# Optimization experiments

Measured on AMD Instinct MI355X. Metric: run time of the kernel, lower is better.

## Reference

```python
import jax, jax.numpy as jnp
import numpy as np

B, S, D = 2, 2048, 1024
H = 16
HD = D // H  # head_dim = 64
EPS = 1e-5


def _layernorm(x, g, b):
    mu = jnp.mean(x, axis=-1, keepdims=True)
    var = jnp.mean(jnp.square(x - mu), axis=-1, keepdims=True)
    return (x - mu) * jax.lax.rsqrt(var + EPS) * g + b


def setup_inputs() -> dict:
    key = jax.random.key(0)
    ks = jax.random.split(key, 6)
    # Xavier-normal-ish init for projection weights (torch Linear layout: [out, in])
    std = float(np.sqrt(2.0 / (D + D)))
    return {
        "query": jax.random.normal(ks[0], (B, S, D), dtype=jnp.float32),
        "q_w": jax.random.normal(ks[1], (D, D), dtype=jnp.float32) * std,
        "q_b": jnp.zeros((D,), jnp.float32),
        "k_w": jax.random.normal(ks[2], (D, D), dtype=jnp.float32) * std,
        "k_b": jnp.zeros((D,), jnp.float32),
        "v_w": jax.random.normal(ks[3], (D, D), dtype=jnp.float32) * std,
        "v_b": jnp.zeros((D,), jnp.float32),
        "o_w": jax.random.normal(ks[4], (D, D), dtype=jnp.float32) * std,
        "o_b": jnp.zeros((D,), jnp.float32),
        "q_ln_g": jnp.ones((HD,), jnp.float32),
        "q_ln_b": jnp.zeros((HD,), jnp.float32),
        "k_ln_g": jnp.ones((HD,), jnp.float32),
        "k_ln_b": jnp.zeros((HD,), jnp.float32),
    }


def reference(query, q_w, q_b, k_w, k_b, v_w, v_b, o_w, o_b,
              q_ln_g, q_ln_b, k_ln_g, k_ln_b) -> jnp.ndarray:
    # Self-attention: key = value = query
    q = query @ q_w.T + q_b           # [B, S, D]
    k = query @ k_w.T + k_b
    v = query @ v_w.T + v_b
    q = q.reshape(B, S, H, HD)
    k = k.reshape(B, S, H, HD)
    v = v.reshape(B, S, H, HD)
    # Per-head QK LayerNorm (ViT-22B stabilization)
    q = _layernorm(q, q_ln_g, q_ln_b)
    k = _layernorm(k, k_ln_g, k_ln_b)
    scale = 1.0 / jnp.sqrt(jnp.asarray(HD, q.dtype))
    attn = jnp.einsum("bqhd,bkhd->bhqk", q, k) * scale  # [B, H, Sq, Skv]
    attn = jax.nn.softmax(attn, axis=-1)
    out = jnp.einsum("bhqk,bkhd->bqhd", attn, v)        # [B, Sq, H, HD]
    out = out.reshape(B, S, D)
    return out @ o_w.T + o_b
```

## Files before the change

kernel.cpp:

```cpp
#include <hip/hip_runtime.h>
#include <hip/hip_bf16.h>

typedef float f32x4 __attribute__((ext_vector_type(4)));
typedef __bf16 bf16x8 __attribute__((ext_vector_type(8)));
typedef unsigned short ushort8 __attribute__((ext_vector_type(8)));
typedef unsigned short ushort4e __attribute__((ext_vector_type(4)));

#define SEQ 2048
#define LOG2E 1.4426950408889634f

__device__ __forceinline__ unsigned short f2bf(float f) {
    unsigned int u = __builtin_bit_cast(unsigned int, f);
    unsigned int r = (u + 0x7FFFu + ((u >> 16) & 1u)) >> 16;
    return (unsigned short)r;
}

__device__ __forceinline__ void gload_lds16(const unsigned short* g, unsigned short* l) {
    __builtin_amdgcn_global_load_lds(
        (const __attribute__((address_space(1))) unsigned int*)g,
        (__attribute__((address_space(3))) unsigned int*)l, 16, 0, 0);
}

__global__ __launch_bounds__(256) void conv_bf16(
    const float* __restrict__ s0, const float* __restrict__ s1,
    const float* __restrict__ s2, const float* __restrict__ s3,
    const float* __restrict__ s4,
    unsigned short* __restrict__ d0, unsigned short* __restrict__ d1,
    unsigned short* __restrict__ d2, unsigned short* __restrict__ d3,
    unsigned short* __restrict__ d4)
{
    const int seg = blockIdx.y;
    const float* s = seg == 0 ? s0 : seg == 1 ? s1 : seg == 2 ? s2 : seg == 3 ? s3 : s4;
    unsigned short* d = seg == 0 ? d0 : seg == 1 ? d1 : seg == 2 ? d2 : seg == 3 ? d3 : d4;
    const int n = seg == 0 ? (4096 * 1024) : (1024 * 1024);
    const int i = (blockIdx.x * 256 + threadIdx.x) * 8;
    if (i >= n) return;
    float4 a = *(const float4*)(s + i);
    float4 b = *(const float4*)(s + i + 4);
    ushort8 o;
    o[0] = f2bf(a.x); o[1] = f2bf(a.y); o[2] = f2bf(a.z); o[3] = f2bf(a.w);
    o[4] = f2bf(b.x); o[5] = f2bf(b.y); o[6] = f2bf(b.z); o[7] = f2bf(b.w);
    *(ushort8*)(d + i) = o;
}

__global__ __launch_bounds__(256) void gemm_bf16(
    const unsigned short* __restrict__ A,
    const unsigned short* __restrict__ W0, const unsigned short* __restrict__ W1,
    const unsigned short* __restrict__ W2,
    const float* __restrict__ b0, const float* __restrict__ b1, const float* __restrict__ b2,
    const float* __restrict__ ln_g0, const float* __restrict__ ln_b0,
    const float* __restrict__ ln_g1, const float* __restrict__ ln_b1,
    unsigned short* __restrict__ qn, unsigned short* __restrict__ kn,
    unsigned short* __restrict__ vt,
    float* __restrict__ Cout, int fixed_mode)
{
    const int z = fixed_mode < 0 ? (int)blockIdx.z : fixed_mode;
    const unsigned short* W = (z == 1) ? W1 : (z == 2) ? W2 : W0;
    const float* bias = (z == 1) ? b1 : (z == 2) ? b2 : b0;

    const int bm = blockIdx.y * 128;
    const int bn = blockIdx.x * 128;

    __shared__ unsigned short As[128 * 64];
    __shared__ unsigned short Bs[128 * 64];

    const int t    = threadIdx.x;
    const int lane = t & 63;
    const int wid  = t >> 6;
    const int l15  = lane & 15;
    const int lhi  = lane >> 4;
    const int wm   = (wid >> 1) * 64;
    const int wn   = (wid & 1) * 64;

    const int schunk = (lane & 7) ^ ((lane >> 3) & 7);
    const unsigned short* Ag = A + (size_t)(bm + (lane >> 3)) * 1024 + schunk * 8;
    const unsigned short* Wg = W + (size_t)(bn + (lane >> 3)) * 1024 + schunk * 8;

    f32x4 acc[4][4];
#pragma unroll
    for (int i = 0; i < 4; ++i)
#pragma unroll
        for (int j = 0; j < 4; ++j) acc[i][j] = (f32x4)0.f;

#pragma unroll 1
    for (int kt = 0; kt < 1024; kt += 64) {
        __syncthreads();
#pragma unroll
        for (int c = 0; c < 4; ++c) {
            const int ch = wid * 4 + c;
            gload_lds16(Ag + (size_t)ch * 8 * 1024 + kt, &As[ch * 512]);
            gload_lds16(Wg + (size_t)ch * 8 * 1024 + kt, &Bs[ch * 512]);
        }
        __syncthreads();
#pragma unroll
        for (int kk = 0; kk < 2; ++kk) {
            const int rchunk = ((kk * 4 + lhi) ^ (l15 & 7)) * 8;
            bf16x8 af[4], bw[4];
#pragma unroll
            for (int mi = 0; mi < 4; ++mi)
                af[mi] = __builtin_bit_cast(bf16x8,
                    *(const ushort8*)(&As[(wm + mi * 16 + l15) * 64 + rchunk]));
#pragma unroll
            for (int ni = 0; ni < 4; ++ni)
                bw[ni] = __builtin_bit_cast(bf16x8,
                    *(const ushort8*)(&Bs[(wn + ni * 16 + l15) * 64 + rchunk]));
#pragma unroll
            for (int mi = 0; mi < 4; ++mi)
#pragma unroll
                for (int ni = 0; ni < 4; ++ni)
                    acc[mi][ni] = __builtin_amdgcn_mfma_f32_16x16x32_bf16(af[mi], bw[ni], acc[mi][ni], 0, 0, 0);
        }
    }
    __syncthreads();

    if (z == 3) {
#pragma unroll
        for (int ni = 0; ni < 4; ++ni) {
            const int col = bn + wn + ni * 16 + l15;
            const float bv = bias[col];
#pragma unroll
            for (int mi = 0; mi < 4; ++mi) {
                const int row = bm + wm + mi * 16 + lhi * 4;
#pragma unroll
                for (int r = 0; r < 4; ++r)
                    Cout[(size_t)(row + r) * 1024 + col] = acc[mi][ni][r] + bv;
            }
        }
        return;
    }

    unsigned short* stg = ((wid & 2) ? Bs : As) + (wid & 1) * 4096;
    const int h = (bn + wn) >> 6;

    if (z == 2) {
        float biasv[4];
#pragma unroll
        for (int ni = 0; ni < 4; ++ni) biasv[ni] = bias[bn + wn + ni * 16 + l15];
#pragma unroll
        for (int mi = 0; mi < 4; ++mi)
#pragma unroll
            for (int ni = 0; ni < 4; ++ni)
#pragma unroll
                for (int r = 0; r < 4; ++r)
                    stg[(ni * 16 + l15) * 64 + 32 * (mi >> 1) + lhi * 8 + 2 * r + (mi & 1)] =
                        f2bf(acc[mi][ni][r] + biasv[ni]);
        __builtin_amdgcn_s_waitcnt(0);
        const int srow0 = bm + wm;
        const int b = srow0 >> 11, sbase = srow0 & 2047;
#pragma unroll
        for (int i = 0; i < 8; ++i) {
            const int dl = i * 8 + (lane >> 3);
            const ushort8 v = *(const ushort8*)(&stg[dl * 64 + (((lane & 7) ^ (dl & 7)) * 8)]);
            *(ushort8*)(&vt[((size_t)((b * 16 + h) * 64 + dl)) * 2048 + sbase + (lane & 7) * 8]) = v;
        }
        return;
    }

    const float* g  = (z == 0) ? ln_g0 : ln_g1;
    const float* bb = (z == 0) ? ln_b0 : ln_b1;
    unsigned short* outp = (z == 0) ? qn : kn;
    const float scale = (z == 0) ? 0.125f * LOG2E : 1.0f;
    const int sxor = (z == 1) ? 7 : 0;
    float gv[4], bbv[4], biasv[4];
#pragma unroll
    for (int ni = 0; ni < 4; ++ni) {
        const int d = ni * 16 + l15;
        gv[ni] = g[d]; bbv[ni] = bb[d]; biasv[ni] = bias[bn + wn + d];
    }
#pragma unroll
    for (int mi = 0; mi < 4; ++mi) {
#pragma unroll
        for (int r = 0; r < 4; ++r) {
            float x0 = acc[mi][0][r] + biasv[0];
            float x1 = acc[mi][1][r] + biasv[1];
            float x2 = acc[mi][2][r] + biasv[2];
            float x3 = acc[mi][3][r] + biasv[3];
            float sum = (x0 + x1) + (x2 + x3);
#pragma unroll
            for (int off = 1; off < 16; off <<= 1) sum += __shfl_xor(sum, off);
            const float mean = sum * (1.f / 64.f);
            const float d0 = x0 - mean, d1 = x1 - mean, d2 = x2 - mean, d3 = x3 - mean;
            float vs = (d0 * d0 + d1 * d1) + (d2 * d2 + d3 * d3);
#pragma unroll
            for (int off = 1; off < 16; off <<= 1) vs += __shfl_xor(vs, off);
            const float rstd = rsqrtf(vs * (1.f / 64.f) + 1e-5f);
            const int rl = mi * 16 + lhi * 4 + r;
            stg[rl * 64 +  0 + l15] = f2bf((d0 * rstd * gv[0] + bbv[0]) * scale);
            stg[rl * 64 + 16 + l15] = f2bf((d1 * rstd * gv[1] + bbv[1]) * scale);
            stg[rl * 64 + 32 + l15] = f2bf((d2 * rstd * gv[2] + bbv[2]) * scale);
            stg[rl * 64 + 48 + l15] = f2bf((d3 * rstd * gv[3] + bbv[3]) * scale);
        }
    }
    __builtin_amdgcn_s_waitcnt(0);
#pragma unroll
    for (int i = 0; i < 8; ++i) {
        const int rl  = i * 8 + (lane >> 3);
        const int srow = bm + wm + rl;
        const int b = srow >> 11, s = srow & 2047;
        const ushort8 v = *(const ushort8*)(&stg[rl * 64 + (((lane & 7) ^ (rl & sxor)) * 8)]);
        *(ushort8*)(&outp[((size_t)((b * 16 + h) * 2048 + s)) * 64 + (lane & 7) * 8]) = v;
    }
}

__global__ __launch_bounds__(512, 4) void attn(
    const unsigned short* __restrict__ qn, const unsigned short* __restrict__ kn,
    const unsigned short* __restrict__ vt, unsigned short* __restrict__ o)
{
    __shared__ unsigned short Ks[4][64 * 64];
    __shared__ unsigned short Vs[4][64 * 64];
    __shared__ unsigned short Ps[128 * 64];

    const int tid  = threadIdx.x;
    const int lane = tid & 63;
    const int w    = tid >> 6;
    const int l15  = lane & 15;
    const int lhi  = lane >> 4;

    const int bh = blockIdx.x;
    const int q0 = blockIdx.y * 128;

    const unsigned short* qrp = qn + ((size_t)bh * SEQ + q0 + w * 16 + l15) * 64 + lhi * 8;
    const bf16x8 aq0 = __builtin_bit_cast(bf16x8, *(const ushort8*)(qrp));
    const bf16x8 aq1 = __builtin_bit_cast(bf16x8, *(const ushort8*)(qrp + 32));

    const unsigned short* kg = kn + ((size_t)bh * SEQ + w * 8 + (lane >> 3)) * 64 + (lane & 7) * 8;
    const unsigned short* vg = vt + ((size_t)bh * 64 + w * 8 + (lane >> 3)) * 2048 + (lane & 7) * 8;

    f32x4 oacc[4];
#pragma unroll
    for (int nd = 0; nd < 4; ++nd) oacc[nd] = (f32x4)0.f;
    float l_part[4];
#pragma unroll
    for (int i = 0; i < 4; ++i) l_part[i] = 0.f;
    f32x4 mneg = (f32x4)100.f;

    f32x4 sacc[4];

    auto QK = [&](const unsigned short* kb) {
        __builtin_amdgcn_s_setprio(1);
#pragma unroll
        for (int ni = 0; ni < 4; ++ni) {
            const int krow = ni * 16 + l15;
            const bf16x8 bk = __builtin_bit_cast(bf16x8,
                *(const ushort8*)(&kb[krow * 64 + ((lhi ^ (krow & 7)) * 8)]));
            sacc[ni] = __builtin_amdgcn_mfma_f32_16x16x32_bf16(aq0, bk, mneg, 0, 0, 0);
        }
#pragma unroll
        for (int ni = 0; ni < 4; ++ni) {
            const int krow = ni * 16 + l15;
            const bf16x8 bk = __builtin_bit_cast(bf16x8,
                *(const ushort8*)(&kb[krow * 64 + (((4 + lhi) ^ (krow & 7)) * 8)]));
            sacc[ni] = __builtin_amdgcn_mfma_f32_16x16x32_bf16(aq1, bk, sacc[ni], 0, 0, 0);
        }
        __builtin_amdgcn_s_setprio(0);
    };

    gload_lds16(kg,                    &Ks[0][w * 512]);
    gload_lds16(vg,                    &Vs[0][w * 512]);
    gload_lds16(kg + (size_t)64 * 64,  &Ks[1][w * 512]);
    gload_lds16(vg + 64,               &Vs[1][w * 512]);
    __builtin_amdgcn_sched_barrier(0);
    asm volatile("s_waitcnt vmcnt(2)" ::: "memory");
    asm volatile("s_barrier" ::: "memory");
    QK(&Ks[0][0]);

#pragma unroll 4
    for (int t = 0; t < 32; ++t) {
        if (t < 30) {
            gload_lds16(kg + (size_t)(t + 2) * 64 * 64, &Ks[(t + 2) & 3][w * 512]);
            gload_lds16(vg + (t + 2) * 64,              &Vs[(t + 2) & 3][w * 512]);
        }
        __builtin_amdgcn_sched_barrier(0);

        float tmax[4];
#pragma unroll
        for (int r = 0; r < 4; ++r)
            tmax[r] = fmaxf(fmaxf(sacc[0][r], sacc[1][r]), fmaxf(sacc[2][r], sacc[3][r]));
        const float dmax = fmaxf(fmaxf(tmax[0], tmax[1]), fmaxf(tmax[2], tmax[3]));
        if (!__all(dmax <= 8.0f)) {
#pragma unroll
            for (int r = 0; r < 4; ++r) {
                float tm = tmax[r];
#pragma unroll
                for (int off = 1; off < 16; off <<= 1) tm = fmaxf(tm, __shfl_xor(tm, off));
                const float delta = fmaxf(tm, 0.f);
                const float alpha = __builtin_amdgcn_exp2f(-delta);
                mneg[r] -= delta;
                l_part[r] *= alpha;
#pragma unroll
                for (int nd = 0; nd < 4; ++nd) oacc[nd][r] *= alpha;
#pragma unroll
                for (int ni = 0; ni < 4; ++ni) sacc[ni][r] -= delta;
            }
        }
#pragma unroll
        for (int r = 0; r < 4; ++r) {
            const float p0 = __builtin_amdgcn_exp2f(sacc[0][r]);
            const float p1 = __builtin_amdgcn_exp2f(sacc[1][r]);
            const float p2 = __builtin_amdgcn_exp2f(sacc[2][r]);
            const float p3 = __builtin_amdgcn_exp2f(sacc[3][r]);
            l_part[r] += (p0 + p1) + (p2 + p3);
            unsigned int pk0, pk1;
            asm("v_cvt_pk_bf16_f32 %0, %1, %2" : "=v"(pk0) : "v"(p0), "v"(p1));
            asm("v_cvt_pk_bf16_f32 %0, %1, %2" : "=v"(pk1) : "v"(p2), "v"(p3));
            const int prow = w * 16 + lhi * 4 + r;
            const int rs7  = prow & 7;
            *(unsigned int*)(&Ps[prow * 64 + (((l15 >> 2) ^ rs7) * 8) + 2 * (l15 & 3)]) = pk0;
            *(unsigned int*)(&Ps[prow * 64 + (((4 + (l15 >> 2)) ^ rs7) * 8) + 2 * (l15 & 3)]) = pk1;
        }

        if (t < 31) {
            if (t < 30) { asm volatile("s_waitcnt vmcnt(2)" ::: "memory"); }
            else        { asm volatile("s_waitcnt vmcnt(0)" ::: "memory"); }
            asm volatile("s_barrier" ::: "memory");
            QK(&Ks[(t + 1) & 3][0]);
        }

        __builtin_amdgcn_s_setprio(1);
#pragma unroll
        for (int kk = 0; kk < 2; ++kk) {
            const int arow = w * 16 + l15;
            const bf16x8 ap = __builtin_bit_cast(bf16x8,
                *(const ushort8*)(&Ps[arow * 64 + (((kk * 4 + lhi) ^ (arow & 7)) * 8)]));
#pragma unroll
            for (int nd = 0; nd < 4; ++nd) {
                const int vrow = nd * 16 + l15;
                const bf16x8 bv = __builtin_bit_cast(bf16x8,
                    *(const ushort8*)(&Vs[t & 3][vrow * 64 + (((kk * 4 + lhi) ^ (vrow & 7)) * 8)]));
                oacc[nd] = __builtin_amdgcn_mfma_f32_16x16x32_bf16(ap, bv, oacc[nd], 0, 0, 0);
            }
        }
        __builtin_amdgcn_s_setprio(0);
    }

    const int b = bh >> 4, h = bh & 15;
#pragma unroll
    for (int r = 0; r < 4; ++r) {
        float ls = l_part[r];
#pragma unroll
        for (int off = 1; off < 16; off <<= 1) ls += __shfl_xor(ls, off);
        const float inv = 1.f / ls;
        const int qrow = q0 + w * 16 + lhi * 4 + r;
        const size_t base = ((size_t)(b * SEQ + qrow) * 16 + h) * 64;
#pragma unroll
        for (int nd = 0; nd < 4; ++nd)
            o[base + nd * 16 + l15] = f2bf(oacc[nd][r] * inv);
    }
}

extern "C" void kernel_launch(void* const* d_in, const int* in_sizes, int n_in,
                              void* d_out, int out_size, void* d_ws, size_t ws_size,
                              hipStream_t stream)
{
    const float* query  = (const float*)d_in[0];
    const float* q_w    = (const float*)d_in[1];
    const float* q_b    = (const float*)d_in[2];
    const float* k_w    = (const float*)d_in[3];
    const float* k_b    = (const float*)d_in[4];
    const float* v_w    = (const float*)d_in[5];
    const float* v_b    = (const float*)d_in[6];
    const float* o_w    = (const float*)d_in[7];
    const float* o_b    = (const float*)d_in[8];
    const float* q_ln_g = (const float*)d_in[9];
    const float* q_ln_b = (const float*)d_in[10];
    const float* k_ln_g = (const float*)d_in[11];
    const float* k_ln_b = (const float*)d_in[12];

    char* ws = (char*)d_ws;
    unsigned short* qbf = (unsigned short*)(ws);
    unsigned short* wq  = (unsigned short*)(ws + (8ull  << 20));
    unsigned short* wk  = (unsigned short*)(ws + (10ull << 20));
    unsigned short* wv  = (unsigned short*)(ws + (12ull << 20));
    unsigned short* wo  = (unsigned short*)(ws + (14ull << 20));
    unsigned short* qnb = (unsigned short*)(ws + (16ull << 20));
    unsigned short* knb = (unsigned short*)(ws + (24ull << 20));
    unsigned short* vtb = (unsigned short*)(ws + (32ull << 20));
    unsigned short* ofb = (unsigned short*)(ws + (40ull << 20));

    conv_bf16<<<dim3(2048, 5), 256, 0, stream>>>(query, q_w, k_w, v_w, o_w,
                                                 qbf, wq, wk, wv, wo);

    dim3 g1(8, 32, 3);
    gemm_bf16<<<g1, 256, 0, stream>>>(qbf, wq, wk, wv, q_b, k_b, v_b,
                                      q_ln_g, q_ln_b, k_ln_g, k_ln_b,
                                      qnb, knb, vtb, nullptr, -1);

    dim3 g3(32, 16);
    attn<<<g3, 512, 0, stream>>>(qnb, knb, vtb, ofb);

    dim3 g4(8, 32, 1);
    gemm_bf16<<<g4, 256, 0, stream>>>(ofb, wo, wo, wo, o_b, o_b, o_b,
                                      nullptr, nullptr, nullptr, nullptr,
                                      nullptr, nullptr, nullptr, (float*)d_out, 3);
}
```

Baseline: 129.5 us.

## Shrink attention tiles to 64 queries and 32-key steps with 256 threads

The attention kernel now uses 256-thread blocks covering 64 query rows instead of 512 threads and 128 rows, and walks the keys in 32-key steps instead of 64. K, V and P shared buffers shrink to match, and the V load and P swizzle are redone so each half of a 64-column V row lands in alternating buffers. The grid doubles to 1024 blocks, which gives more blocks per CU and better latency hiding through lower LDS use. In exchange each block reloads K and V more often, the loop has twice as many iterations and barriers, and there are fewer MFMAs between each softmax step.

```diff
diff --git a/kernel.cpp b/kernel.cpp
--- a/kernel.cpp
+++ b/kernel.cpp
@@ -4,7 +4,6 @@
 typedef float f32x4 __attribute__((ext_vector_type(4)));
 typedef __bf16 bf16x8 __attribute__((ext_vector_type(8)));
 typedef unsigned short ushort8 __attribute__((ext_vector_type(8)));
-typedef unsigned short ushort4e __attribute__((ext_vector_type(4)));
 
 #define SEQ 2048
 #define LOG2E 1.4426950408889634f
@@ -202,13 +201,13 @@
     }
 }
 
-__global__ __launch_bounds__(512, 4) void attn(
+__global__ __launch_bounds__(256, 4) void attn(
     const unsigned short* __restrict__ qn, const unsigned short* __restrict__ kn,
     const unsigned short* __restrict__ vt, unsigned short* __restrict__ o)
 {
-    __shared__ unsigned short Ks[4][64 * 64];
-    __shared__ unsigned short Vs[4][64 * 64];
-    __shared__ unsigned short Ps[128 * 64];
+    __shared__ unsigned short Ks[4][32 * 64];
+    __shared__ unsigned short Vs[4][64 * 32];
+    __shared__ unsigned short Ps[64 * 32];
 
     const int tid  = threadIdx.x;
     const int lane = tid & 63;
@@ -217,14 +216,20 @@
     const int lhi  = lane >> 4;
 
     const int bh = blockIdx.x;
-    const int q0 = blockIdx.y * 128;
+    const int q0 = blockIdx.y * 64;
 
     const unsigned short* qrp = qn + ((size_t)bh * SEQ + q0 + w * 16 + l15) * 64 + lhi * 8;
     const bf16x8 aq0 = __builtin_bit_cast(bf16x8, *(const ushort8*)(qrp));
     const bf16x8 aq1 = __builtin_bit_cast(bf16x8, *(const ushort8*)(qrp + 32));
 
     const unsigned short* kg = kn + ((size_t)bh * SEQ + w * 8 + (lane >> 3)) * 64 + (lane & 7) * 8;
-    const unsigned short* vg = vt + ((size_t)bh * 64 + w * 8 + (lane >> 3)) * 2048 + (lane & 7) * 8;
+
+    const int vx   = lane & 3;
+    const int vswz = (lane >> 3) & 3;
+    const int vrot = (lane >> 2) & 7;
+    const unsigned short* vg = vt + ((size_t)bh * 64 + w * 16 + (lane >> 2)) * 2048;
+    const int off_even = (((vx ^ vswz) + 0) ^ vrot) * 8;
+    const int off_odd  = (((vx ^ vswz) + 4) ^ vrot) * 8;
 
     f32x4 oacc[4];
 #pragma unroll
@@ -234,19 +239,19 @@
     for (int i = 0; i < 4; ++i) l_part[i] = 0.f;
     f32x4 mneg = (f32x4)100.f;
 
-    f32x4 sacc[4];
+    f32x4 sacc[2];
 
     auto QK = [&](const unsigned short* kb) {
         __builtin_amdgcn_s_setprio(1);
 #pragma unroll
-        for (int ni = 0; ni < 4; ++ni) {
+        for (int ni = 0; ni < 2; ++ni) {
             const int krow = ni * 16 + l15;
             const bf16x8 bk = __builtin_bit_cast(bf16x8,
                 *(const ushort8*)(&kb[krow * 64 + ((lhi ^ (krow & 7)) * 8)]));
             sacc[ni] = __builtin_amdgcn_mfma_f32_16x16x32_bf16(aq0, bk, mneg, 0, 0, 0);
         }
 #pragma unroll
-        for (int ni = 0; ni < 4; ++ni) {
+        for (int ni = 0; ni < 2; ++ni) {
             const int krow = ni * 16 + l15;
             const bf16x8 bk = __builtin_bit_cast(bf16x8,
                 *(const ushort8*)(&kb[krow * 64 + (((4 + lhi) ^ (krow & 7)) * 8)]));
@@ -255,27 +260,28 @@
         __builtin_amdgcn_s_setprio(0);
     };
 
-    gload_lds16(kg,                    &Ks[0][w * 512]);
-    gload_lds16(vg,                    &Vs[0][w * 512]);
-    gload_lds16(kg + (size_t)64 * 64,  &Ks[1][w * 512]);
-    gload_lds16(vg + 64,               &Vs[1][w * 512]);
+    gload_lds16(kg,            &Ks[0][w * 512]);
+    gload_lds16(vg + off_even, &Vs[0][w * 512]);
+    gload_lds16(kg + 2048,     &Ks[1][w * 512]);
+    gload_lds16(vg + off_odd,  &Vs[1][w * 512]);
     __builtin_amdgcn_sched_barrier(0);
     asm volatile("s_waitcnt vmcnt(2)" ::: "memory");
     asm volatile("s_barrier" ::: "memory");
     QK(&Ks[0][0]);
 
 #pragma unroll 4
-    for (int t = 0; t < 32; ++t) {
-        if (t < 30) {
-            gload_lds16(kg + (size_t)(t + 2) * 64 * 64, &Ks[(t + 2) & 3][w * 512]);
-            gload_lds16(vg + (t + 2) * 64,              &Vs[(t + 2) & 3][w * 512]);
+    for (int t = 0; t < 64; ++t) {
+        if (t < 62) {
+            gload_lds16(kg + (size_t)(t + 2) * 2048, &Ks[(t + 2) & 3][w * 512]);
+            gload_lds16(vg + ((t + 2) >> 1) * 64 + (((t + 2) & 1) ? off_odd : off_even),
+                        &Vs[(t + 2) & 3][w * 512]);
         }
         __builtin_amdgcn_sched_barrier(0);
 
         float tmax[4];
 #pragma unroll
         for (int r = 0; r < 4; ++r)
-            tmax[r] = fmaxf(fmaxf(sacc[0][r], sacc[1][r]), fmaxf(sacc[2][r], sacc[3][r]));
+            tmax[r] = fmaxf(sacc[0][r], sacc[1][r]);
         const float dmax = fmaxf(fmaxf(tmax[0], tmax[1]), fmaxf(tmax[2], tmax[3]));
         if (!__all(dmax <= 8.0f)) {
 #pragma unroll
@@ -289,44 +295,39 @@
                 l_part[r] *= alpha;
 #pragma unroll
                 for (int nd = 0; nd < 4; ++nd) oacc[nd][r] *= alpha;
-#pragma unroll
-                for (int ni = 0; ni < 4; ++ni) sacc[ni][r] -= delta;
+                sacc[0][r] -= delta;
+                sacc[1][r] -= delta;
             }
         }
 #pragma unroll
         for (int r = 0; r < 4; ++r) {
             const float p0 = __builtin_amdgcn_exp2f(sacc[0][r]);
             const float p1 = __builtin_amdgcn_exp2f(sacc[1][r]);
-            const float p2 = __builtin_amdgcn_exp2f(sacc[2][r]);
-            const float p3 = __builtin_amdgcn_exp2f(sacc[3][r]);
-            l_part[r] += (p0 + p1) + (p2 + p3);
-            unsigned int pk0, pk1;
+            l_part[r] += p0 + p1;
+            unsigned int pk0;
             asm("v_cvt_pk_bf16_f32 %0, %1, %2" : "=v"(pk0) : "v"(p0), "v"(p1));
-            asm("v_cvt_pk_bf16_f32 %0, %1, %2" : "=v"(pk1) : "v"(p2), "v"(p3));
             const int prow = w * 16 + lhi * 4 + r;
-            const int rs7  = prow & 7;
-            *(unsigned int*)(&Ps[prow * 64 + (((l15 >> 2) ^ rs7) * 8) + 2 * (l15 & 3)]) = pk0;
-            *(unsigned int*)(&Ps[prow * 64 + (((4 + (l15 >> 2)) ^ rs7) * 8) + 2 * (l15 & 3)]) = pk1;
-        }
-
-        if (t < 31) {
-            if (t < 30) { asm volatile("s_waitcnt vmcnt(2)" ::: "memory"); }
+            *(unsigned int*)(&Ps[prow * 32 + (((l15 >> 2) ^ ((prow >> 1) & 3)) * 8) + 2 * (l15 & 3)]) = pk0;
+        }
+
+        if (t < 63) {
+            if (t < 62) { asm volatile("s_waitcnt vmcnt(2)" ::: "memory"); }
             else        { asm volatile("s_waitcnt vmcnt(0)" ::: "memory"); }
             asm volatile("s_barrier" ::: "memory");
             QK(&Ks[(t + 1) & 3][0]);
         }
 
         __builtin_amdgcn_s_setprio(1);
-#pragma unroll
-        for (int kk = 0; kk < 2; ++kk) {
+        {
             const int arow = w * 16 + l15;
+            const int pswz = (l15 >> 1) & 3;
             const bf16x8 ap = __builtin_bit_cast(bf16x8,
-                *(const ushort8*)(&Ps[arow * 64 + (((kk * 4 + lhi) ^ (arow & 7)) * 8)]));
+                *(const ushort8*)(&Ps[arow * 32 + ((lhi ^ pswz) * 8)]));
 #pragma unroll
             for (int nd = 0; nd < 4; ++nd) {
                 const int vrow = nd * 16 + l15;
                 const bf16x8 bv = __builtin_bit_cast(bf16x8,
-                    *(const ushort8*)(&Vs[t & 3][vrow * 64 + (((kk * 4 + lhi) ^ (vrow & 7)) * 8)]));
+                    *(const ushort8*)(&Vs[t & 3][vrow * 32 + ((lhi ^ pswz) * 8)]));
                 oacc[nd] = __builtin_amdgcn_mfma_f32_16x16x32_bf16(ap, bv, oacc[nd], 0, 0, 0);
             }
         }
@@ -385,8 +386,8 @@
                                       q_ln_g, q_ln_b, k_ln_g, k_ln_b,
                                       qnb, knb, vtb, nullptr, -1);
 
-    dim3 g3(32, 16);
-    attn<<<g3, 512, 0, stream>>>(qnb, knb, vtb, ofb);
+    dim3 g3(32, 32);
+    attn<<<g3, 256, 0, stream>>>(qnb, knb, vtb, ofb);
 
     dim3 g4(8, 32, 1);
     gemm_bf16<<<g4, 256, 0, stream>>>(ofb, wo, wo, wo, o_b, o_b, o_b,
```

Measured after the change: 138.2 us. +6.7%, slower.
